# Optimization experiments

Measured on AMD Instinct MI355X. Metric: run time of the kernel, lower is better.

Reference implementation:

```python
import jax, jax.numpy as jnp
import numpy as np

B, N, M, C = 4, 768, 768, 128
K_NN, K1_NN = 16, 8
NUM_KEYPOINTS = 256
NN_MARGIN = 0.7


def pairwise_distance_batch(x, y):
    # x: (B,C,N), y: (B,C,M) -> squared euclidean distance map (B,N,M)
    xx = jnp.sum(x * x, axis=1)[:, :, None]
    yy = jnp.sum(y * y, axis=1)[:, None, :]
    return xx + yy - 2.0 * jnp.einsum('bcn,bcm->bnm', x, y)


def discriminator(knn_distance, src_knn_distance, w1, b1, w2, b2, w3, b3, w4, b4):
    # inlier-evaluation weight function: pointwise MLP over (B,N,k,6), max-pool over k, MLP -> sigmoid weight (B,1,N)
    x = jnp.concatenate([knn_distance, src_knn_distance], axis=-1)  # (B,N,k,6)
    h = jax.nn.relu(jnp.einsum('bnkc,oc->bnko', x, w1) + b1)
    h = jax.nn.relu(jnp.einsum('bnko,po->bnkp', h, w2) + b2)
    g = h.max(axis=2)  # (B,N,64) pool over neighbors
    g = jax.nn.relu(jnp.einsum('bnp,qp->bnq', g, w3) + b3)
    w = jax.nn.sigmoid(jnp.einsum('bnq,rq->bnr', g, w4) + b4)  # (B,N,1)
    return w.transpose(0, 2, 1)  # (B,1,N)


def compute_rigid_transformation(src, src_corr, weight):
    # weighted Kabsch/SVD rigid fit. src/src_corr: (B,3,N), weight: (B,1,N)
    w = weight / (jnp.sum(weight, axis=2, keepdims=True) + 1e-8)
    src_mean = jnp.sum(src * w, axis=2, keepdims=True)
    corr_mean = jnp.sum(src_corr * w, axis=2, keepdims=True)
    src_c = (src - src_mean) * w
    corr_c = src_corr - corr_mean
    H = jnp.einsum('bin,bjn->bij', src_c, corr_c)  # (B,3,3)
    U, S, Vt = jnp.linalg.svd(H)
    V = Vt.transpose(0, 2, 1)
    det = jnp.linalg.det(jnp.einsum('bij,bkj->bik', V, U))  # det(V U^T)
    d = jnp.stack([jnp.ones_like(det), jnp.ones_like(det), det], axis=-1)  # (B,3)
    R = jnp.einsum('bij,bj,bkj->bik', V, d, U)
    t = corr_mean - jnp.einsum('bij,bjk->bik', R, src_mean)  # (B,3,1)
    return R, t


def _forward(src, tgt, src_embedding, tgt_embedding, src_idx, k, src_knn, i, tgt_knn, src_idx1, idx2, k1,
             w1, b1, w2, b2, w3, b3, w4, b4, num_keypoints, nn_margin):
    Bs, _, Ns = src.shape
    Ms = tgt.shape[2]
    dist = pairwise_distance_batch(src_embedding, tgt_embedding)  # (B,N,M)
    scores = jax.nn.softmax(-dist, axis=2)
    # neighborhood consensus: sum_{a>=1,c>=1} scores[b, nbr_src(i,a), nbr_tgt(j,c)] / (k1-1)
    S1 = scores.reshape(Bs * Ns, Ms)[src_idx1].reshape(Bs, Ns, k1, Ms)  # gather src-neighbor rows
    A = jnp.sum(S1[:, :, 1:, :], axis=2)  # (B,N,M), drop self (a=0)
    idx2c = idx2[:, :, 1:]  # (B,M,k1-1), drop self (c=0)
    consensus = jax.vmap(lambda a, idx: jnp.sum(a[:, idx], axis=-1))(A, idx2c) / (k1 - 1)  # (B,N,M)
    src_knn_scores = nn_margin - consensus
    refined = jnp.exp(src_knn_scores) * dist
    matching = jax.nn.softmax(-refined, axis=2)  # refined matching map (B,N,M)
    src_corr = jnp.einsum('bcm,bnm->bcn', tgt, matching)  # soft correspondences (B,3,N)
    src_corr_t = src_corr.transpose(0, 2, 1)  # (B,N,3)
    src_knn_corr = src_corr_t.reshape(Bs * Ns, 3)[src_idx].reshape(Bs, Ns, k, 3)
    knn_distance = src_corr_t[:, :, None, :] - src_knn_corr  # (B,N,k,3)
    src_knn_distance = src.transpose(0, 2, 1)[:, :, None, :] - src_knn
    weight = discriminator(knn_distance, src_knn_distance, w1, b1, w2, b2, w3, b3, w4, b4)  # (B,1,N)
    R, t = compute_rigid_transformation(src, src_corr, weight)
    _, topk_idx = jax.lax.top_k(weight[:, 0, :], num_keypoints)  # (B,K)
    bidx = jnp.arange(Bs)[:, None]
    bc = jnp.broadcast_to(topk_idx[:, None, :], (Bs, 3, num_keypoints))
    src_keypoints = jnp.take_along_axis(src, bc, axis=2)  # (B,3,K)
    tgt_keypoints = jnp.take_along_axis(src_corr, bc, axis=2)
    idx_tgt_corr = jnp.argmax(matching, axis=-1)  # (B,N)
    kp_corr = jnp.take_along_axis(idx_tgt_corr, topk_idx, axis=1)  # (B,K)
    keypoints_one_hot = jax.nn.one_hot(kp_corr, Ms, dtype=matching.dtype)  # (B,K,M)
    pred_scores = matching[bidx, topk_idx]  # (B,K,M)
    loss_scl = jnp.mean(jnp.sum(-jnp.log(pred_scores + 1e-15) * keypoints_one_hot, axis=-1))
    tgt_keypoints_knn = knn_distance[bidx, topk_idx].transpose(0, 3, 1, 2)  # (B,3,K,k)
    src_transformed = jnp.einsum('bij,bjn->bin', R, src) + t
    st = src_transformed.transpose(0, 2, 1)  # (B,N,3)
    st_knn_corr = st.reshape(Bs * Ns, 3)[src_idx].reshape(Bs, Ns, k, 3)
    knn_distance2 = st[:, :, None, :] - st_knn_corr
    src_keypoints_knn = knn_distance2[bidx, topk_idx].transpose(0, 3, 1, 2)  # (B,3,K,k)
    return (R, t.reshape(Bs, 3), src_keypoints, tgt_keypoints, src_keypoints_knn, tgt_keypoints_knn, loss_scl)


def setup_inputs() -> dict:
    key = jax.random.key(0)
    ks = jax.random.split(key, 12)
    src = jax.random.normal(ks[0], (B, 3, N), jnp.float32)
    tgt = jax.random.normal(ks[1], (B, 3, M), jnp.float32)
    src_embedding = jax.random.normal(ks[2], (B, C, N), jnp.float32)
    tgt_embedding = jax.random.normal(ks[3], (B, C, M), jnp.float32)
    # knn index lists; first neighbor is the point itself (matching the [:,:,1:] self-exclusion slices)
    idxk = jax.random.randint(ks[4], (B, N, K_NN), 0, N).at[:, :, 0].set(jnp.arange(N)[None, :])
    idxk1 = jax.random.randint(ks[5], (B, N, K1_NN), 0, N).at[:, :, 0].set(jnp.arange(N)[None, :])
    idx2 = jax.random.randint(ks[6], (B, M, K1_NN), 0, M).at[:, :, 0].set(jnp.arange(M)[None, :])
    off = jnp.arange(B)[:, None, None] * N
    src_idx = (idxk + off).reshape(-1)   # flat indices into (B*N) rows
    src_idx1 = (idxk1 + off).reshape(-1)
    bidx = jnp.arange(B)[:, None, None]
    src_knn = src.transpose(0, 2, 1)[bidx, idxk]   # (B,N,k,3) coords of neighbors
    tgt_knn = tgt.transpose(0, 2, 1)[bidx, idx2]   # (B,M,k1,3) (unused by forward, kept for signature fidelity)
    s = 0.1
    w1 = jax.random.normal(ks[7], (64, 6), jnp.float32) * s
    w2 = jax.random.normal(ks[8], (64, 64), jnp.float32) * s
    w3 = jax.random.normal(ks[9], (32, 64), jnp.float32) * s
    w4 = jax.random.normal(ks[10], (1, 32), jnp.float32) * s
    return {"src": src, "tgt": tgt, "src_embedding": src_embedding, "tgt_embedding": tgt_embedding,
            "src_idx": src_idx, "k": K_NN, "src_knn": src_knn, "i": 0, "tgt_knn": tgt_knn,
            "src_idx1": src_idx1, "idx2": idx2, "k1": K1_NN,
            "w1": w1, "b1": jnp.zeros((64,), jnp.float32), "w2": w2, "b2": jnp.zeros((64,), jnp.float32),
            "w3": w3, "b3": jnp.zeros((32,), jnp.float32), "w4": w4, "b4": jnp.zeros((1,), jnp.float32),
            "num_keypoints": NUM_KEYPOINTS, "nn_margin": NN_MARGIN}


def reference(src, tgt, src_embedding, tgt_embedding, src_idx, k, src_knn, i, tgt_knn, src_idx1, idx2, k1,
              w1, b1, w2, b2, w3, b3, w4, b4, num_keypoints, nn_margin):
    return _forward(src, tgt, src_embedding, tgt_embedding, src_idx, k, src_knn, i, tgt_knn, src_idx1, idx2, k1,
                    w1, b1, w2, b2, w3, b3, w4, b4, num_keypoints, nn_margin)
```

## Files before the change

kernel.cpp:

```cpp
#include <hip/hip_runtime.h>
#include <hip/hip_bf16.h>
#include <math.h>

#define BB 4
#define NN 768
#define MM 768
#define CC 128
#define KK 16
#define KK1 8
#define NKP 256

#define OFF_R    0
#define OFF_T    36
#define OFF_SK   48
#define OFF_TK   3120
#define OFF_SKK  6192
#define OFF_TKK  55344
#define OFF_LOSS 104496

__global__ __launch_bounds__(256) void dist_k(const float* __restrict__ xe,
                                              const float* __restrict__ ye,
                                              float* __restrict__ dist) {
    __shared__ float xt[CC * 64];
    __shared__ float yt[CC * 64];
    __shared__ float nx[64];
    __shared__ float ny[64];
    int b = blockIdx.z, n0 = blockIdx.y * 64, m0 = blockIdx.x * 64;
    int tid = threadIdx.x;
    for (int i = tid; i < CC * 16; i += 256) {
        int c = i >> 4, v = i & 15;
        ((float4*)xt)[c * 16 + v] = ((const float4*)(xe + (size_t)(b * CC + c) * NN + n0))[v];
        ((float4*)yt)[c * 16 + v] = ((const float4*)(ye + (size_t)(b * CC + c) * MM + m0))[v];
    }
    __syncthreads();
    if (tid < 64) {
        float s = 0.f;
        for (int c = 0; c < CC; c++) { float v = xt[c * 64 + tid]; s += v * v; }
        nx[tid] = s;
    } else if (tid < 128) {
        int v0 = tid - 64;
        float s = 0.f;
        for (int c = 0; c < CC; c++) { float v = yt[c * 64 + v0]; s += v * v; }
        ny[v0] = s;
    }
    int mi = (tid & 15) * 4;
    int ni = (tid >> 4) * 4;
    float acc[16];
    for (int k = 0; k < 16; k++) acc[k] = 0.f;
    for (int c = 0; c < CC; c++) {
        float4 xv = *(const float4*)&xt[c * 64 + ni];
        float4 yv = *(const float4*)&yt[c * 64 + mi];
        acc[0]  += xv.x * yv.x; acc[1]  += xv.x * yv.y; acc[2]  += xv.x * yv.z; acc[3]  += xv.x * yv.w;
        acc[4]  += xv.y * yv.x; acc[5]  += xv.y * yv.y; acc[6]  += xv.y * yv.z; acc[7]  += xv.y * yv.w;
        acc[8]  += xv.z * yv.x; acc[9]  += xv.z * yv.y; acc[10] += xv.z * yv.z; acc[11] += xv.z * yv.w;
        acc[12] += xv.w * yv.x; acc[13] += xv.w * yv.y; acc[14] += xv.w * yv.z; acc[15] += xv.w * yv.w;
    }
    __syncthreads();
    float ny0 = ny[mi], ny1 = ny[mi + 1], ny2 = ny[mi + 2], ny3 = ny[mi + 3];
    for (int i = 0; i < 4; i++) {
        float nxi = nx[ni + i];
        float4 o;
        o.x = nxi + ny0 - 2.f * acc[i * 4 + 0];
        o.y = nxi + ny1 - 2.f * acc[i * 4 + 1];
        o.z = nxi + ny2 - 2.f * acc[i * 4 + 2];
        o.w = nxi + ny3 - 2.f * acc[i * 4 + 3];
        *(float4*)&dist[((size_t)b * NN + n0 + ni + i) * MM + m0 + mi] = o;
    }
}

__global__ __launch_bounds__(256) void scores_k(const float* __restrict__ dist,
                                                float* __restrict__ scores) {
    __shared__ float red[4];
    int r = blockIdx.x, tid = threadIdx.x;
    int lane = tid & 63, wv = tid >> 6;
    const float* dr = dist + (size_t)r * MM;
    float v[3]; float mn = 1e30f;
    for (int q = 0; q < 3; q++) { v[q] = dr[tid + 256 * q]; mn = fminf(mn, v[q]); }
    for (int off = 32; off >= 1; off >>= 1) mn = fminf(mn, __shfl_down(mn, off));
    if (lane == 0) red[wv] = mn;
    __syncthreads();
    mn = fminf(fminf(red[0], red[1]), fminf(red[2], red[3]));
    __syncthreads();
    float e[3], z = 0.f;
    for (int q = 0; q < 3; q++) { e[q] = expf(mn - v[q]); z += e[q]; }
    for (int off = 32; off >= 1; off >>= 1) z += __shfl_down(z, off);
    if (lane == 0) red[wv] = z;
    __syncthreads();
    z = red[0] + red[1] + red[2] + red[3];
    float inv = 1.0f / z;
    for (int q = 0; q < 3; q++) scores[(size_t)r * MM + tid + 256 * q] = e[q] * inv;
}

__global__ __launch_bounds__(256) void match_k(const float* __restrict__ dist,
                                               const float* __restrict__ scores,
                                               const int* __restrict__ src_idx1,
                                               const int* __restrict__ idx2,
                                               const float* __restrict__ tgt,
                                               const float* __restrict__ nn_margin_p,
                                               float* __restrict__ src_corr,
                                               float* __restrict__ mmax) {
    __shared__ float Arow[MM];
    __shared__ float red[4];
    __shared__ float red4[16];
    int r = blockIdx.x, tid = threadIdx.x;
    int lane = tid & 63, wv = tid >> 6;
    int b = r / NN, n = r % NN;
    int rows[KK1 - 1];
    for (int j = 0; j < KK1 - 1; j++) rows[j] = src_idx1[r * KK1 + 1 + j];
    for (int q = 0; q < 3; q++) {
        int m = tid + 256 * q;
        float a = 0.f;
        for (int j = 0; j < KK1 - 1; j++) a += scores[(size_t)rows[j] * MM + m];
        Arow[m] = a;
    }
    __syncthreads();
    float marg = nn_margin_p[0];
    const float* drow = dist + (size_t)r * MM;
    float rv[3]; float mn = 1e30f;
    for (int q = 0; q < 3; q++) {
        int m = tid + 256 * q;
        const int4* ip = (const int4*)(idx2 + ((size_t)b * MM + m) * KK1);
        int4 i0 = ip[0], i1 = ip[1];
        float cons = Arow[i0.y] + Arow[i0.z] + Arow[i0.w] +
                     Arow[i1.x] + Arow[i1.y] + Arow[i1.z] + Arow[i1.w];
        rv[q] = expf(marg - cons * (1.0f / (KK1 - 1))) * drow[m];
        mn = fminf(mn, rv[q]);
    }
    for (int off = 32; off >= 1; off >>= 1) mn = fminf(mn, __shfl_down(mn, off));
    if (lane == 0) red[wv] = mn;
    __syncthreads();
    mn = fminf(fminf(red[0], red[1]), fminf(red[2], red[3]));
    float z = 0.f, s0 = 0.f, s1 = 0.f, s2 = 0.f;
    const float* t0 = tgt + (size_t)b * 3 * MM;
    for (int q = 0; q < 3; q++) {
        int m = tid + 256 * q;
        float e = expf(mn - rv[q]);
        z += e;
        s0 += e * t0[m];
        s1 += e * t0[MM + m];
        s2 += e * t0[2 * MM + m];
    }
    for (int off = 32; off >= 1; off >>= 1) {
        z += __shfl_down(z, off); s0 += __shfl_down(s0, off);
        s1 += __shfl_down(s1, off); s2 += __shfl_down(s2, off);
    }
    if (lane == 0) { red4[wv * 4] = z; red4[wv * 4 + 1] = s0; red4[wv * 4 + 2] = s1; red4[wv * 4 + 3] = s2; }
    __syncthreads();
    if (tid == 0) {
        float zt = red4[0] + red4[4] + red4[8] + red4[12];
        float s0t = red4[1] + red4[5] + red4[9] + red4[13];
        float s1t = red4[2] + red4[6] + red4[10] + red4[14];
        float s2t = red4[3] + red4[7] + red4[11] + red4[15];
        float inv = 1.0f / zt;
        src_corr[(size_t)(b * 3 + 0) * NN + n] = s0t * inv;
        src_corr[(size_t)(b * 3 + 1) * NN + n] = s1t * inv;
        src_corr[(size_t)(b * 3 + 2) * NN + n] = s2t * inv;
        mmax[r] = inv;
    }
}

__global__ __launch_bounds__(256) void disc_k(const float* __restrict__ src,
                                              const float* __restrict__ src_corr,
                                              const float* __restrict__ src_knn,
                                              const int* __restrict__ src_idx,
                                              const float* __restrict__ w1, const float* __restrict__ b1,
                                              const float* __restrict__ w2, const float* __restrict__ b2,
                                              const float* __restrict__ w3, const float* __restrict__ b3,
                                              const float* __restrict__ w4, const float* __restrict__ b4,
                                              float* __restrict__ knnD, float* __restrict__ wgt) {
    __shared__ float w1s[64 * 7];
    __shared__ float w2s[64 * 65];
    __shared__ float w3s[32 * 65];
    __shared__ float xs[4][16 * 6];
    __shared__ float h1s[4][16 * 64];
    __shared__ float gs[4][64];
    int tid = threadIdx.x;
    for (int i = tid; i < 64 * 6; i += 256) w1s[(i / 6) * 7 + (i % 6)] = w1[i];
    for (int i = tid; i < 64 * 64; i += 256) w2s[(i / 64) * 65 + (i % 64)] = w2[i];
    for (int i = tid; i < 32 * 64; i += 256) w3s[(i / 64) * 65 + (i % 64)] = w3[i];
    int w = tid >> 6, l = tid & 63;
    int r = blockIdx.x * 4 + w;
    int b = r / NN, n = r % NN;
    if (l < KK) {
        int j = l;
        int f = src_idx[r * KK + j];
        int fb = f / NN, fn = f % NN;
        for (int c = 0; c < 3; c++) {
            float scn = src_corr[(size_t)(b * 3 + c) * NN + n];
            float kd = scn - src_corr[(size_t)(fb * 3 + c) * NN + fn];
            xs[w][j * 6 + c] = kd;
            knnD[((size_t)r * KK + j) * 3 + c] = kd;
            float sd = src[(size_t)(b * 3 + c) * NN + n] - src_knn[((size_t)r * KK + j) * 3 + c];
            xs[w][j * 6 + 3 + c] = sd;
        }
    }
    __syncthreads();
    float bb1 = b1[l];
    for (int k = 0; k < KK; k++) {
        float h = bb1;
        for (int c = 0; c < 6; c++) h += xs[w][k * 6 + c] * w1s[l * 7 + c];
        h1s[w][k * 64 + l] = h > 0.f ? h : 0.f;
    }
    __syncthreads();
    float bb2 = b2[l];
    float acc2[KK];
    for (int k = 0; k < KK; k++) acc2[k] = bb2;
    for (int o4 = 0; o4 < 16; o4++) {
        float wa = w2s[l * 65 + o4 * 4 + 0];
        float wb = w2s[l * 65 + o4 * 4 + 1];
        float wc = w2s[l * 65 + o4 * 4 + 2];
        float wd = w2s[l * 65 + o4 * 4 + 3];
        for (int k = 0; k < KK; k++) {
            float4 h = *(const float4*)&h1s[w][k * 64 + o4 * 4];
            acc2[k] += h.x * wa + h.y * wb + h.z * wc + h.w * wd;
        }
    }
    float gm = 0.f;
    for (int k = 0; k < KK; k++) gm = fmaxf(gm, acc2[k]);
    gs[w][l] = gm;
    __syncthreads();
    float val = 0.f;
    if (l < 32) {
        float h = b3[l];
        for (int o = 0; o < 64; o++) h += gs[w][o] * w3s[l * 65 + o];
        h = h > 0.f ? h : 0.f;
        val = h * w4[l];
    }
    for (int off = 32; off >= 1; off >>= 1) val += __shfl_down(val, off);
    if (l == 0) wgt[r] = 1.0f / (1.0f + expf(-(val + b4[0])));
}

__global__ __launch_bounds__(256) void bsumrigid_k(const float* __restrict__ src,
                                                   const float* __restrict__ src_corr,
                                                   const float* __restrict__ wgt,
                                                   float* __restrict__ out,
                                                   float* __restrict__ Rws, float* __restrict__ tws,
                                                   float* __restrict__ lossAcc) {
    __shared__ double redd[BB * 16];
    int tid = threadIdx.x;
    int wv = tid >> 6, lane = tid & 63;
    int b = wv;
    double acc[16];
    for (int k = 0; k < 16; k++) acc[k] = 0.0;
    for (int n = lane; n < NN; n += 64) {
        double wvv = wgt[b * NN + n];
        double s[3], q[3];
        for (int i = 0; i < 3; i++) {
            s[i] = src[(size_t)(b * 3 + i) * NN + n];
            q[i] = src_corr[(size_t)(b * 3 + i) * NN + n];
        }
        acc[0] += wvv;
        for (int i = 0; i < 3; i++) acc[1 + i] += wvv * s[i];
        for (int j = 0; j < 3; j++) acc[4 + j] += wvv * q[j];
        for (int i = 0; i < 3; i++)
            for (int j = 0; j < 3; j++) acc[7 + i * 3 + j] += wvv * s[i] * q[j];
    }
    for (int k = 0; k < 16; k++)
        for (int off = 32; off >= 1; off >>= 1) acc[k] += __shfl_down(acc[k], off);
    if (lane == 0)
        for (int k = 0; k < 16; k++) redd[b * 16 + k] = acc[k];
    __syncthreads();
    if (tid == 0) { lossAcc[0] = 0.f; ((int*)lossAcc)[1] = 0; }
    if (tid >= BB) return;
    int bb = tid;
    const double* S = redd + bb * 16;
    double T = S[0], D = T + 1e-8;
    double sm[3], cm[3];
    for (int i = 0; i < 3; i++) { sm[i] = S[1 + i] / D; cm[i] = S[4 + i] / D; }
    double fac = 2.0 - T / D;
    double H[3][3];
    for (int i = 0; i < 3; i++)
        for (int j = 0; j < 3; j++) H[i][j] = S[7 + i * 3 + j] / D - sm[i] * cm[j] * fac;
    double Sxx = H[0][0], Sxy = H[0][1], Sxz = H[0][2];
    double Syx = H[1][0], Syy = H[1][1], Syz = H[1][2];
    double Szx = H[2][0], Szy = H[2][1], Szz = H[2][2];
    double A[4][4];
    A[0][0] = Sxx + Syy + Szz; A[0][1] = Syz - Szy;        A[0][2] = Szx - Sxz;        A[0][3] = Sxy - Syx;
    A[1][0] = A[0][1];         A[1][1] = Sxx - Syy - Szz;  A[1][2] = Sxy + Syx;        A[1][3] = Szx + Sxz;
    A[2][0] = A[0][2];         A[2][1] = A[1][2];          A[2][2] = -Sxx + Syy - Szz; A[2][3] = Syz + Szy;
    A[3][0] = A[0][3];         A[3][1] = A[1][3];          A[3][2] = A[2][3];          A[3][3] = -Sxx - Syy + Szz;
    double V[4][4] = {{1,0,0,0},{0,1,0,0},{0,0,1,0},{0,0,0,1}};
    for (int sweep = 0; sweep < 15; sweep++) {
        double off = A[0][1]*A[0][1] + A[0][2]*A[0][2] + A[0][3]*A[0][3]
                   + A[1][2]*A[1][2] + A[1][3]*A[1][3] + A[2][3]*A[2][3];
        if (off < 1e-26) break;
        for (int p = 0; p < 3; p++) {
            for (int q = p + 1; q < 4; q++) {
                double apq = A[p][q];
                if (fabs(apq) < 1e-60) continue;
                double theta = 0.5 * (A[q][q] - A[p][p]) / apq;
                double t = (theta >= 0 ? 1.0 : -1.0) / (fabs(theta) + sqrt(theta * theta + 1.0));
                double c = 1.0 / sqrt(t * t + 1.0), s = t * c;
                for (int k = 0; k < 4; k++) {
                    double akp = A[k][p], akq = A[k][q];
                    A[k][p] = c * akp - s * akq; A[k][q] = s * akp + c * akq;
                }
                for (int k = 0; k < 4; k++) {
                    double apk = A[p][k], aqk = A[q][k];
                    A[p][k] = c * apk - s * aqk; A[q][k] = s * apk + c * aqk;
                }
                for (int k = 0; k < 4; k++) {
                    double vkp = V[k][p], vkq = V[k][q];
                    V[k][p] = c * vkp - s * vkq; V[k][q] = s * vkp + c * vkq;
                }
            }
        }
    }
    int best = 0;
    for (int k = 1; k < 4; k++) if (A[k][k] > A[best][best]) best = k;
    double qw = V[0][best], qx = V[1][best], qy = V[2][best], qz = V[3][best];
    double nq = sqrt(qw * qw + qx * qx + qy * qy + qz * qz);
    qw /= nq; qx /= nq; qy /= nq; qz /= nq;
    double R[3][3];
    R[0][0] = 1 - 2 * (qy * qy + qz * qz); R[0][1] = 2 * (qx * qy - qw * qz); R[0][2] = 2 * (qx * qz + qw * qy);
    R[1][0] = 2 * (qx * qy + qw * qz); R[1][1] = 1 - 2 * (qx * qx + qz * qz); R[1][2] = 2 * (qy * qz - qw * qx);
    R[2][0] = 2 * (qx * qz - qw * qy); R[2][1] = 2 * (qy * qz + qw * qx); R[2][2] = 1 - 2 * (qx * qx + qy * qy);
    for (int i = 0; i < 3; i++)
        for (int j = 0; j < 3; j++) {
            out[OFF_R + bb * 9 + i * 3 + j] = (float)R[i][j];
            Rws[bb * 9 + i * 3 + j] = (float)R[i][j];
        }
    for (int i = 0; i < 3; i++) {
        double tv = cm[i] - (R[i][0] * sm[0] + R[i][1] * sm[1] + R[i][2] * sm[2]);
        out[OFF_T + bb * 3 + i] = (float)tv;
        tws[bb * 3 + i] = (float)tv;
    }
}

__global__ __launch_bounds__(256) void topk_k(const float* __restrict__ wgt, int* __restrict__ topk,
                                              const float* __restrict__ src, const float* __restrict__ Rws,
                                              const float* __restrict__ tws, float* __restrict__ st) {
    __shared__ float wl[NN];
    int b = blockIdx.y, tid = threadIdx.x;
    for (int i = tid; i < NN; i += 256) wl[i] = wgt[b * NN + i];
    __syncthreads();
    int i = blockIdx.x * 64 + (tid >> 2);
    int q = tid & 3;
    float v = wl[i];
    int rank = 0;
    for (int t = 0; t < NN / 4; t++) {
        int j = q + 4 * t;
        float u = wl[j];
        rank += (u > v) || (u == v && j < i);
    }
    rank += __shfl_down(rank, 2, 4);
    rank += __shfl_down(rank, 1, 4);
    if (q == 0 && rank < NKP) topk[b * NKP + rank] = i;
    int gid = (b * (NN / 64) + blockIdx.x) * 256 + tid;
    if (gid < BB * 3 * NN) {
        int n = gid % NN; int bi = gid / NN; int b2 = bi / 3, ii = bi % 3;
        const float* Rb = Rws + b2 * 9 + ii * 3;
        const float* sb = src + (size_t)b2 * 3 * NN;
        st[gid] = Rb[0] * sb[n] + Rb[1] * sb[NN + n] + Rb[2] * sb[2 * NN + n] + tws[b2 * 3 + ii];
    }
}

__global__ __launch_bounds__(256) void gather_k(const float* __restrict__ src,
                                                const float* __restrict__ src_corr,
                                                const float* __restrict__ knnD,
                                                const float* __restrict__ st,
                                                const int* __restrict__ src_idx,
                                                const int* __restrict__ topk,
                                                const float* __restrict__ mmax,
                                                float* __restrict__ lossAcc,
                                                float* __restrict__ out) {
    __shared__ float lred[4];
    int tid = threadIdx.x;
    int t = blockIdx.x * 256 + tid;
    int j = t % KK; int br = t / KK; int r = br % NKP; int b = br / NKP;
    int idx = topk[b * NKP + r];
    int rr = b * NN + idx;
    for (int c = 0; c < 3; c++)
        out[OFF_TKK + (size_t)((b * 3 + c) * NKP + r) * KK + j] = knnD[((size_t)rr * KK + j) * 3 + c];
    int f = src_idx[rr * KK + j];
    int fb = f / NN, fn = f % NN;
    for (int c = 0; c < 3; c++)
        out[OFF_SKK + (size_t)((b * 3 + c) * NKP + r) * KK + j] =
            st[(size_t)(b * 3 + c) * NN + idx] - st[(size_t)(fb * 3 + c) * NN + fn];
    float term = 0.f;
    if (j == 0) {
        for (int c = 0; c < 3; c++) {
            out[OFF_SK + (b * 3 + c) * NKP + r] = src[(size_t)(b * 3 + c) * NN + idx];
            out[OFF_TK + (b * 3 + c) * NKP + r] = src_corr[(size_t)(b * 3 + c) * NN + idx];
        }
        term = -logf(mmax[rr] + 1e-15f);
    }
    int lane = tid & 63, wv = tid >> 6;
    for (int off = 32; off >= 1; off >>= 1) term += __shfl_down(term, off);
    if (lane == 0) lred[wv] = term;
    __syncthreads();
    if (tid == 0) {
        float bsum = lred[0] + lred[1] + lred[2] + lred[3];
        atomicAdd(&lossAcc[0], bsum);
        __threadfence();
        int old = atomicAdd((int*)&lossAcc[1], 1);
        if (old == (int)gridDim.x - 1) {
            float fin = atomicAdd(&lossAcc[0], 0.f);
            out[OFF_LOSS] = fin / (float)(BB * NKP);
        }
    }
}

extern "C" void kernel_launch(void* const* d_in, const int* in_sizes, int n_in,
                              void* d_out, int out_size, void* d_ws, size_t ws_size,
                              hipStream_t stream) {
    (void)in_sizes; (void)n_in; (void)out_size; (void)ws_size;
    const float* src      = (const float*)d_in[0];
    const float* tgt      = (const float*)d_in[1];
    const float* se       = (const float*)d_in[2];
    const float* te       = (const float*)d_in[3];
    const int*   src_idx  = (const int*)d_in[4];
    const float* src_knn  = (const float*)d_in[6];
    const int*   src_idx1 = (const int*)d_in[9];
    const int*   idx2     = (const int*)d_in[10];
    const float* w1 = (const float*)d_in[12];
    const float* b1 = (const float*)d_in[13];
    const float* w2 = (const float*)d_in[14];
    const float* b2 = (const float*)d_in[15];
    const float* w3 = (const float*)d_in[16];
    const float* b3 = (const float*)d_in[17];
    const float* w4 = (const float*)d_in[18];
    const float* b4 = (const float*)d_in[19];
    const float* nn_margin = (const float*)d_in[21];
    float* out = (float*)d_out;

    float* ws = (float*)d_ws;
    float* dist     = ws;
    float* scores   = dist + (size_t)BB * NN * MM;
    float* src_corr = scores + (size_t)BB * NN * MM;
    float* mmax     = src_corr + BB * 3 * NN;
    float* knnD     = mmax + BB * NN;
    float* wgt      = knnD + (size_t)BB * NN * KK * 3;
    float* Rws      = wgt + BB * NN;
    float* tws      = Rws + BB * 9;
    float* st       = tws + BB * 3;
    int*   topk     = (int*)(st + BB * 3 * NN);
    float* lossAcc  = (float*)(topk + BB * NKP);

    dist_k<<<dim3(MM / 64, NN / 64, BB), 256, 0, stream>>>(se, te, dist);
    scores_k<<<BB * NN, 256, 0, stream>>>(dist, scores);
    match_k<<<BB * NN, 256, 0, stream>>>(dist, scores, src_idx1, idx2, tgt, nn_margin,
                                         src_corr, mmax);
    disc_k<<<BB * NN / 4, 256, 0, stream>>>(src, src_corr, src_knn, src_idx,
                                            w1, b1, w2, b2, w3, b3, w4, b4, knnD, wgt);
    bsumrigid_k<<<1, 256, 0, stream>>>(src, src_corr, wgt, out, Rws, tws, lossAcc);
    topk_k<<<dim3(NN / 64, BB), 256, 0, stream>>>(wgt, topk, src, Rws, tws, st);
    gather_k<<<BB * NKP * KK / 256, 256, 0, stream>>>(src, src_corr, knnD, st,
                                                      src_idx, topk, mmax, lossAcc, out);
}
```

Baseline: 194.4 us.

## Drop materialized softmax scores; recompute from row stats and fuse rigid with topk

The score matrix is no longer written out. A stats kernel stores each row's min and inverse partition sum, and the match kernel recomputes the neighbor softmax values from dist with exp, using one wavefront per row and float4 loads. The rigid fit and the top-k ranking now run as separate blocks of one launch, and the transformed source points are computed inside the gather kernel instead of in a separate pass. This removes a full B*N*M write and read plus one launch, at the cost of seven extra exps per element in the match kernel.

```diff
diff --git a/kernel.cpp b/kernel.cpp
--- a/kernel.cpp
+++ b/kernel.cpp
@@ -43,8 +43,7 @@
         for (int c = 0; c < CC; c++) { float v = yt[c * 64 + v0]; s += v * v; }
         ny[v0] = s;
     }
-    int mi = (tid & 15) * 4;
-    int ni = (tid >> 4) * 4;
+    int mi = (tid & 15) * 4, ni = (tid >> 4) * 4;
     float acc[16];
     for (int k = 0; k < 16; k++) acc[k] = 0.f;
     for (int c = 0; c < CC; c++) {
@@ -68,93 +67,111 @@
     }
 }
 
-__global__ __launch_bounds__(256) void scores_k(const float* __restrict__ dist,
-                                                float* __restrict__ scores) {
-    __shared__ float red[4];
-    int r = blockIdx.x, tid = threadIdx.x;
+__global__ __launch_bounds__(256) void stats_k(const float* __restrict__ dist,
+                                               float* __restrict__ rowstats) {
+    int tid = threadIdx.x;
     int lane = tid & 63, wv = tid >> 6;
+    int r = blockIdx.x * 4 + wv;
     const float* dr = dist + (size_t)r * MM;
-    float v[3]; float mn = 1e30f;
-    for (int q = 0; q < 3; q++) { v[q] = dr[tid + 256 * q]; mn = fminf(mn, v[q]); }
+    float4 v4[3];
+    float mn = 1e30f;
+    for (int q = 0; q < 3; q++) {
+        v4[q] = *(const float4*)&dr[256 * q + lane * 4];
+        mn = fminf(mn, fminf(fminf(v4[q].x, v4[q].y), fminf(v4[q].z, v4[q].w)));
+    }
     for (int off = 32; off >= 1; off >>= 1) mn = fminf(mn, __shfl_down(mn, off));
-    if (lane == 0) red[wv] = mn;
-    __syncthreads();
-    mn = fminf(fminf(red[0], red[1]), fminf(red[2], red[3]));
-    __syncthreads();
-    float e[3], z = 0.f;
-    for (int q = 0; q < 3; q++) { e[q] = expf(mn - v[q]); z += e[q]; }
+    mn = __shfl(mn, 0);
+    float z = 0.f;
+    for (int q = 0; q < 3; q++) {
+        z += expf(mn - v4[q].x) + expf(mn - v4[q].y) + expf(mn - v4[q].z) + expf(mn - v4[q].w);
+    }
     for (int off = 32; off >= 1; off >>= 1) z += __shfl_down(z, off);
-    if (lane == 0) red[wv] = z;
-    __syncthreads();
-    z = red[0] + red[1] + red[2] + red[3];
-    float inv = 1.0f / z;
-    for (int q = 0; q < 3; q++) scores[(size_t)r * MM + tid + 256 * q] = e[q] * inv;
+    if (lane == 0) { rowstats[2 * r] = mn; rowstats[2 * r + 1] = 1.0f / z; }
 }
 
 __global__ __launch_bounds__(256) void match_k(const float* __restrict__ dist,
-                                               const float* __restrict__ scores,
+                                               const float* __restrict__ rowstats,
                                                const int* __restrict__ src_idx1,
                                                const int* __restrict__ idx2,
                                                const float* __restrict__ tgt,
                                                const float* __restrict__ nn_margin_p,
                                                float* __restrict__ src_corr,
                                                float* __restrict__ mmax) {
-    __shared__ float Arow[MM];
-    __shared__ float red[4];
-    __shared__ float red4[16];
-    int r = blockIdx.x, tid = threadIdx.x;
+    __shared__ float ArowAll[4 * MM];
+    int tid = threadIdx.x;
     int lane = tid & 63, wv = tid >> 6;
+    int r = blockIdx.x * 4 + wv;
     int b = r / NN, n = r % NN;
+    float* Arow = ArowAll + wv * MM;
     int rows[KK1 - 1];
-    for (int j = 0; j < KK1 - 1; j++) rows[j] = src_idx1[r * KK1 + 1 + j];
-    for (int q = 0; q < 3; q++) {
-        int m = tid + 256 * q;
-        float a = 0.f;
-        for (int j = 0; j < KK1 - 1; j++) a += scores[(size_t)rows[j] * MM + m];
-        Arow[m] = a;
-    }
+    float mnj[KK1 - 1], izj[KK1 - 1];
+    for (int j = 0; j < KK1 - 1; j++) {
+        rows[j] = src_idx1[r * KK1 + 1 + j];
+        mnj[j] = rowstats[2 * rows[j]];
+        izj[j] = rowstats[2 * rows[j] + 1];
+    }
+    float4 a4[3];
+    for (int q = 0; q < 3; q++) a4[q] = make_float4(0.f, 0.f, 0.f, 0.f);
+    for (int j = 0; j < KK1 - 1; j++) {
+        const float* dj = dist + (size_t)rows[j] * MM;
+        float mj = mnj[j], iz = izj[j];
+        for (int q = 0; q < 3; q++) {
+            float4 d = *(const float4*)&dj[256 * q + lane * 4];
+            a4[q].x += expf(mj - d.x) * iz;
+            a4[q].y += expf(mj - d.y) * iz;
+            a4[q].z += expf(mj - d.z) * iz;
+            a4[q].w += expf(mj - d.w) * iz;
+        }
+    }
+    for (int q = 0; q < 3; q++)
+        *(float4*)&Arow[256 * q + lane * 4] = a4[q];
     __syncthreads();
     float marg = nn_margin_p[0];
     const float* drow = dist + (size_t)r * MM;
-    float rv[3]; float mn = 1e30f;
+    float4 rv4[3];
+    float mn = 1e30f;
     for (int q = 0; q < 3; q++) {
-        int m = tid + 256 * q;
-        const int4* ip = (const int4*)(idx2 + ((size_t)b * MM + m) * KK1);
-        int4 i0 = ip[0], i1 = ip[1];
-        float cons = Arow[i0.y] + Arow[i0.z] + Arow[i0.w] +
-                     Arow[i1.x] + Arow[i1.y] + Arow[i1.z] + Arow[i1.w];
-        rv[q] = expf(marg - cons * (1.0f / (KK1 - 1))) * drow[m];
-        mn = fminf(mn, rv[q]);
+        int mbase = 256 * q + lane * 4;
+        float4 d = *(const float4*)&drow[mbase];
+        float rr[4];
+        for (int c = 0; c < 4; c++) {
+            int m = mbase + c;
+            const int4* ip = (const int4*)(idx2 + ((size_t)b * MM + m) * KK1);
+            int4 i0 = ip[0], i1 = ip[1];
+            float cons = Arow[i0.y] + Arow[i0.z] + Arow[i0.w] +
+                         Arow[i1.x] + Arow[i1.y] + Arow[i1.z] + Arow[i1.w];
+            float dc = (c == 0) ? d.x : (c == 1) ? d.y : (c == 2) ? d.z : d.w;
+            rr[c] = expf(marg - cons * (1.0f / (KK1 - 1))) * dc;
+            mn = fminf(mn, rr[c]);
+        }
+        rv4[q] = make_float4(rr[0], rr[1], rr[2], rr[3]);
     }
     for (int off = 32; off >= 1; off >>= 1) mn = fminf(mn, __shfl_down(mn, off));
-    if (lane == 0) red[wv] = mn;
-    __syncthreads();
-    mn = fminf(fminf(red[0], red[1]), fminf(red[2], red[3]));
+    mn = __shfl(mn, 0);
     float z = 0.f, s0 = 0.f, s1 = 0.f, s2 = 0.f;
     const float* t0 = tgt + (size_t)b * 3 * MM;
     for (int q = 0; q < 3; q++) {
-        int m = tid + 256 * q;
-        float e = expf(mn - rv[q]);
-        z += e;
-        s0 += e * t0[m];
-        s1 += e * t0[MM + m];
-        s2 += e * t0[2 * MM + m];
+        int mbase = 256 * q + lane * 4;
+        float4 ta = *(const float4*)&t0[mbase];
+        float4 tb = *(const float4*)&t0[MM + mbase];
+        float4 tc = *(const float4*)&t0[2 * MM + mbase];
+        float4 e4;
+        e4.x = expf(mn - rv4[q].x); e4.y = expf(mn - rv4[q].y);
+        e4.z = expf(mn - rv4[q].z); e4.w = expf(mn - rv4[q].w);
+        z  += e4.x + e4.y + e4.z + e4.w;
+        s0 += e4.x * ta.x + e4.y * ta.y + e4.z * ta.z + e4.w * ta.w;
+        s1 += e4.x * tb.x + e4.y * tb.y + e4.z * tb.z + e4.w * tb.w;
+        s2 += e4.x * tc.x + e4.y * tc.y + e4.z * tc.z + e4.w * tc.w;
     }
     for (int off = 32; off >= 1; off >>= 1) {
         z += __shfl_down(z, off); s0 += __shfl_down(s0, off);
         s1 += __shfl_down(s1, off); s2 += __shfl_down(s2, off);
     }
-    if (lane == 0) { red4[wv * 4] = z; red4[wv * 4 + 1] = s0; red4[wv * 4 + 2] = s1; red4[wv * 4 + 3] = s2; }
-    __syncthreads();
-    if (tid == 0) {
-        float zt = red4[0] + red4[4] + red4[8] + red4[12];
-        float s0t = red4[1] + red4[5] + red4[9] + red4[13];
-        float s1t = red4[2] + red4[6] + red4[10] + red4[14];
-        float s2t = red4[3] + red4[7] + red4[11] + red4[15];
-        float inv = 1.0f / zt;
-        src_corr[(size_t)(b * 3 + 0) * NN + n] = s0t * inv;
-        src_corr[(size_t)(b * 3 + 1) * NN + n] = s1t * inv;
-        src_corr[(size_t)(b * 3 + 2) * NN + n] = s2t * inv;
+    if (lane == 0) {
+        float inv = 1.0f / z;
+        src_corr[(size_t)(b * 3 + 0) * NN + n] = s0 * inv;
+        src_corr[(size_t)(b * 3 + 1) * NN + n] = s1 * inv;
+        src_corr[(size_t)(b * 3 + 2) * NN + n] = s2 * inv;
         mmax[r] = inv;
     }
 }
@@ -230,15 +247,36 @@
     if (l == 0) wgt[r] = 1.0f / (1.0f + expf(-(val + b4[0])));
 }
 
-__global__ __launch_bounds__(256) void bsumrigid_k(const float* __restrict__ src,
+__global__ __launch_bounds__(256) void rigidtopk_k(const float* __restrict__ src,
                                                    const float* __restrict__ src_corr,
                                                    const float* __restrict__ wgt,
                                                    float* __restrict__ out,
                                                    float* __restrict__ Rws, float* __restrict__ tws,
+                                                   int* __restrict__ topk,
                                                    float* __restrict__ lossAcc) {
+    int tid = threadIdx.x;
+    int lane = tid & 63, wv = tid >> 6;
+    if (blockIdx.x < 48) {
+        __shared__ float wl[NN];
+        int job = blockIdx.x;
+        int bx = job % 12, b = job / 12;
+        for (int i = tid; i < NN; i += 256) wl[i] = wgt[b * NN + i];
+        __syncthreads();
+        int i = bx * 64 + (tid >> 2);
+        int q = tid & 3;
+        float v = wl[i];
+        int rank = 0;
+        for (int t = 0; t < NN / 4; t++) {
+            int j = q + 4 * t;
+            float u = wl[j];
+            rank += (u > v) || (u == v && j < i);
+        }
+        rank += __shfl_down(rank, 2, 4);
+        rank += __shfl_down(rank, 1, 4);
+        if (q == 0 && rank < NKP) topk[b * NKP + rank] = i;
+        return;
+    }
     __shared__ double redd[BB * 16];
-    int tid = threadIdx.x;
-    int wv = tid >> 6, lane = tid & 63;
     int b = wv;
     double acc[16];
     for (int k = 0; k < 16; k++) acc[k] = 0.0;
@@ -281,9 +319,9 @@
     A[3][0] = A[0][3];         A[3][1] = A[1][3];          A[3][2] = A[2][3];          A[3][3] = -Sxx - Syy + Szz;
     double V[4][4] = {{1,0,0,0},{0,1,0,0},{0,0,1,0},{0,0,0,1}};
     for (int sweep = 0; sweep < 15; sweep++) {
-        double off = A[0][1]*A[0][1] + A[0][2]*A[0][2] + A[0][3]*A[0][3]
-                   + A[1][2]*A[1][2] + A[1][3]*A[1][3] + A[2][3]*A[2][3];
-        if (off < 1e-26) break;
+        double offd = A[0][1]*A[0][1] + A[0][2]*A[0][2] + A[0][3]*A[0][3]
+                    + A[1][2]*A[1][2] + A[1][3]*A[1][3] + A[2][3]*A[2][3];
+        if (offd < 1e-26) break;
         for (int p = 0; p < 3; p++) {
             for (int q = p + 1; q < 4; q++) {
                 double apq = A[p][q];
@@ -327,45 +365,19 @@
     }
 }
 
-__global__ __launch_bounds__(256) void topk_k(const float* __restrict__ wgt, int* __restrict__ topk,
-                                              const float* __restrict__ src, const float* __restrict__ Rws,
-                                              const float* __restrict__ tws, float* __restrict__ st) {
-    __shared__ float wl[NN];
-    int b = blockIdx.y, tid = threadIdx.x;
-    for (int i = tid; i < NN; i += 256) wl[i] = wgt[b * NN + i];
-    __syncthreads();
-    int i = blockIdx.x * 64 + (tid >> 2);
-    int q = tid & 3;
-    float v = wl[i];
-    int rank = 0;
-    for (int t = 0; t < NN / 4; t++) {
-        int j = q + 4 * t;
-        float u = wl[j];
-        rank += (u > v) || (u == v && j < i);
-    }
-    rank += __shfl_down(rank, 2, 4);
-    rank += __shfl_down(rank, 1, 4);
-    if (q == 0 && rank < NKP) topk[b * NKP + rank] = i;
-    int gid = (b * (NN / 64) + blockIdx.x) * 256 + tid;
-    if (gid < BB * 3 * NN) {
-        int n = gid % NN; int bi = gid / NN; int b2 = bi / 3, ii = bi % 3;
-        const float* Rb = Rws + b2 * 9 + ii * 3;
-        const float* sb = src + (size_t)b2 * 3 * NN;
-        st[gid] = Rb[0] * sb[n] + Rb[1] * sb[NN + n] + Rb[2] * sb[2 * NN + n] + tws[b2 * 3 + ii];
-    }
-}
-
 __global__ __launch_bounds__(256) void gather_k(const float* __restrict__ src,
                                                 const float* __restrict__ src_corr,
                                                 const float* __restrict__ knnD,
-                                                const float* __restrict__ st,
                                                 const int* __restrict__ src_idx,
                                                 const int* __restrict__ topk,
+                                                const float* __restrict__ Rws,
+                                                const float* __restrict__ tws,
                                                 const float* __restrict__ mmax,
                                                 float* __restrict__ lossAcc,
                                                 float* __restrict__ out) {
     __shared__ float lred[4];
     int tid = threadIdx.x;
+    int lane = tid & 63, wv = tid >> 6;
     int t = blockIdx.x * 256 + tid;
     int j = t % KK; int br = t / KK; int r = br % NKP; int b = br / NKP;
     int idx = topk[b * NKP + r];
@@ -374,18 +386,27 @@
         out[OFF_TKK + (size_t)((b * 3 + c) * NKP + r) * KK + j] = knnD[((size_t)rr * KK + j) * 3 + c];
     int f = src_idx[rr * KK + j];
     int fb = f / NN, fn = f % NN;
-    for (int c = 0; c < 3; c++)
-        out[OFF_SKK + (size_t)((b * 3 + c) * NKP + r) * KK + j] =
-            st[(size_t)(b * 3 + c) * NN + idx] - st[(size_t)(fb * 3 + c) * NN + fn];
+    float Rb[9], tb[3], Rf[9], tf[3];
+    for (int c = 0; c < 9; c++) { Rb[c] = Rws[b * 9 + c]; Rf[c] = Rws[fb * 9 + c]; }
+    for (int c = 0; c < 3; c++) { tb[c] = tws[b * 3 + c]; tf[c] = tws[fb * 3 + c]; }
+    float sp[3], sf[3];
+    for (int c = 0; c < 3; c++) {
+        sp[c] = src[(size_t)(b * 3 + c) * NN + idx];
+        sf[c] = src[(size_t)(fb * 3 + c) * NN + fn];
+    }
+    for (int c = 0; c < 3; c++) {
+        float sti = Rb[c*3] * sp[0] + Rb[c*3+1] * sp[1] + Rb[c*3+2] * sp[2] + tb[c];
+        float stf = Rf[c*3] * sf[0] + Rf[c*3+1] * sf[1] + Rf[c*3+2] * sf[2] + tf[c];
+        out[OFF_SKK + (size_t)((b * 3 + c) * NKP + r) * KK + j] = sti - stf;
+    }
     float term = 0.f;
     if (j == 0) {
         for (int c = 0; c < 3; c++) {
-            out[OFF_SK + (b * 3 + c) * NKP + r] = src[(size_t)(b * 3 + c) * NN + idx];
+            out[OFF_SK + (b * 3 + c) * NKP + r] = sp[c];
             out[OFF_TK + (b * 3 + c) * NKP + r] = src_corr[(size_t)(b * 3 + c) * NN + idx];
         }
         term = -logf(mmax[rr] + 1e-15f);
     }
-    int lane = tid & 63, wv = tid >> 6;
     for (int off = 32; off >= 1; off >>= 1) term += __shfl_down(term, off);
     if (lane == 0) lred[wv] = term;
     __syncthreads();
@@ -426,25 +447,23 @@
 
     float* ws = (float*)d_ws;
     float* dist     = ws;
-    float* scores   = dist + (size_t)BB * NN * MM;
-    float* src_corr = scores + (size_t)BB * NN * MM;
+    float* rowstats = dist + (size_t)BB * NN * MM;
+    float* src_corr = rowstats + BB * NN * 2;
     float* mmax     = src_corr + BB * 3 * NN;
     float* knnD     = mmax + BB * NN;
     float* wgt      = knnD + (size_t)BB * NN * KK * 3;
     float* Rws      = wgt + BB * NN;
     float* tws      = Rws + BB * 9;
-    float* st       = tws + BB * 3;
-    int*   topk     = (int*)(st + BB * 3 * NN);
+    int*   topk     = (int*)(tws + BB * 3);
     float* lossAcc  = (float*)(topk + BB * NKP);
 
     dist_k<<<dim3(MM / 64, NN / 64, BB), 256, 0, stream>>>(se, te, dist);
-    scores_k<<<BB * NN, 256, 0, stream>>>(dist, scores);
-    match_k<<<BB * NN, 256, 0, stream>>>(dist, scores, src_idx1, idx2, tgt, nn_margin,
-                                         src_corr, mmax);
+    stats_k<<<BB * NN / 4, 256, 0, stream>>>(dist, rowstats);
+    match_k<<<BB * NN / 4, 256, 0, stream>>>(dist, rowstats, src_idx1, idx2, tgt, nn_margin,
+                                             src_corr, mmax);
     disc_k<<<BB * NN / 4, 256, 0, stream>>>(src, src_corr, src_knn, src_idx,
                                             w1, b1, w2, b2, w3, b3, w4, b4, knnD, wgt);
-    bsumrigid_k<<<1, 256, 0, stream>>>(src, src_corr, wgt, out, Rws, tws, lossAcc);
-    topk_k<<<dim3(NN / 64, BB), 256, 0, stream>>>(wgt, topk, src, Rws, tws, st);
-    gather_k<<<BB * NKP * KK / 256, 256, 0, stream>>>(src, src_corr, knnD, st,
-                                                      src_idx, topk, mmax, lossAcc, out);
-}
+    rigidtopk_k<<<49, 256, 0, stream>>>(src, src_corr, wgt, out, Rws, tws, topk, lossAcc);
+    gather_k<<<BB * NKP * KK / 256, 256, 0, stream>>>(src, src_corr, knnD, src_idx, topk,
+                                                      Rws, tws, mmax, lossAcc, out);
+}
```

Result: faster. 184.7 us (-5.0%).
